# Performance work log

Measured on AMD Instinct MI355X. Metric: run time of the kernel, lower is better.

Reference implementation:

```python
import jax, jax.numpy as jnp
import numpy as np


def setup_inputs() -> dict:
    key = jax.random.key(0)
    ks = jax.random.split(key, 12)
    b, c, h, w = 2, 128, 256, 512          # x: [b,c,h,w], h == d_model
    n_cond, d_cond, d_attn = 512, 512, 256  # single head: d_attn = n_heads*d_head = 256
    return {
        "x": jax.random.normal(ks[0], (b, c, h, w), jnp.float32),
        "v": jax.random.normal(ks[1], (b, n_cond, d_cond), jnp.float32),
        "Wq": jax.random.normal(ks[2], (h, d_attn), jnp.float32) * 0.05,
        "Wk": jax.random.normal(ks[3], (d_cond, d_attn), jnp.float32) * 0.05,
        "Wv": jax.random.normal(ks[4], (d_cond, d_attn), jnp.float32) * 0.05,
        "Wo": jax.random.normal(ks[5], (d_attn, h), jnp.float32) * 0.05,
        "bo": jnp.zeros((h,), jnp.float32),
        "mask_w": jax.random.normal(ks[6], (h,), jnp.float32),  # ConvTranspose2d(1,1,(1,h)) weight, applied to ones -> just the kernel
        "conv_w": jax.random.normal(ks[7], (c, 2 * c, 3, 3), jnp.float32) * 0.02,
        "conv_b": jnp.zeros((c,), jnp.float32),
        "gn_gamma": jnp.ones((c,), jnp.float32),
        "gn_beta": jnp.zeros((c,), jnp.float32),
    }


def reference(x, v, Wq, Wk, Wv, Wo, bo, mask_w, conv_w, conv_b, gn_gamma, gn_beta):
    b, c, h, w = x.shape
    # ---- CrossAttention (note: self.scale defined but never applied in source) ----
    xt = jnp.swapaxes(x, 2, 3)                        # [b,c,w,h]
    q = jnp.einsum("bcwh,hd->bcwd", xt, Wq)           # [b,c,w,d_attn]
    k = jnp.einsum("bnd,de->bne", v, Wk)              # [b,n_cond,d_attn]
    val = jnp.einsum("bnd,de->bne", v, Wv)
    attn = jnp.einsum("bcwd,bnd->bcwn", q, k)         # [b,c,w,n_cond]
    attn = jax.nn.softmax(attn, axis=-1)
    out = jnp.einsum("bcwn,bnd->bcwd", attn, val)     # [b,c,w,d_attn]
    out = jnp.einsum("bcwd,dh->bcwh", out, Wo) + bo   # [b,c,w,h]
    attn_feature = jnp.swapaxes(out, 2, 3)            # [b,c,h,w]

    # ---- NonAdaptiveLearnedMask (eval mode: no Gaussian noise) ----
    sig = jax.nn.sigmoid(mask_w)                      # [h]
    x2 = jnp.broadcast_to(sig[None, :], (b, h))       # [b,h]
    k_keep = int(h * (1.0 - 0.2))                     # p=0.2 hardcoded in module
    topval = jax.lax.top_k(x2, k_keep)[0][:, -1:]     # kth-largest per row [b,1]
    comp = (x2 >= topval).astype(x2.dtype)
    wta = comp * x2                                   # sparsified sigmoid outputs
    slope = 1.0
    probs = jax.nn.sigmoid(slope * wta)
    hard = (probs > 0.5).astype(x2.dtype)             # straight-through binary act
    binary = probs + jax.lax.stop_gradient(hard - probs)  # [b,h]
    binary_mask = jnp.broadcast_to(binary[:, None, None, :], (b, 1, w, h))
    masked_x = jnp.swapaxes(binary_mask * jnp.swapaxes(x, 2, 3), 2, 3)  # [b,c,h,w]

    # ---- conv3x3 on concat + GroupNorm + SiLU ----
    cat = jnp.concatenate([masked_x, attn_feature], axis=1)  # [b,2c,h,w]
    hh = jax.lax.conv_general_dilated(
        cat, conv_w, window_strides=(1, 1), padding="SAME",
        dimension_numbers=("NCHW", "OIHW", "NCHW"))
    hh = hh + conv_b[None, :, None, None]
    g = min(c // 4, 32)
    hr = hh.reshape(b, g, c // g, h, w)
    mean = hr.mean(axis=(2, 3, 4), keepdims=True)
    var = hr.var(axis=(2, 3, 4), keepdims=True)
    hn = ((hr - mean) * jax.lax.rsqrt(var + 1e-6)).reshape(b, c, h, w)
    hn = hn * gn_gamma[None, :, None, None] + gn_beta[None, :, None, None]
    out = hn * jax.nn.sigmoid(hn)  # SiLU
    return (out, binary_mask)
```

## Files before the change

### kernel.cpp

```cpp
#include <hip/hip_runtime.h>
#include <math.h>

#define B      2
#define C      128
#define H      256
#define W      512
#define NCOND  512
#define DCOND  512
#define DATTN  256
#define KKEEP  204

#define WS_CATN   0ull
#define WS_KQ     134742016ull
#define WS_VOT    135266304ull
#define WS_W9     135790592ull
#define WS_BIN    136380416ull
#define WS_ST2    136381440ull

typedef __attribute__((ext_vector_type(8))) short bf16x8;
typedef __attribute__((ext_vector_type(4))) float f32x4;

union U8 { bf16x8 v; ushort u[8]; };

__device__ inline ushort f2bf(float f) {
    union { float f; unsigned u; } v; v.f = f;
    unsigned r = v.u + 0x7fffu + ((v.u >> 16) & 1u);
    return (ushort)(r >> 16);
}

__device__ __forceinline__ void gld16(const ushort* g, void* l) {
    __builtin_amdgcn_global_load_lds(
        (const __attribute__((address_space(1))) unsigned int*)(const void*)g,
        (__attribute__((address_space(3))) unsigned int*)l, 16, 0, 0);
}

__global__ void k_binary(const float* __restrict__ mask_w, float* __restrict__ bin) {
    __shared__ float s[H];
    int t = threadIdx.x;
    float sv = 1.0f / (1.0f + __expf(-mask_w[t]));
    s[t] = sv;
    __syncthreads();
    int cnt = 0;
    for (int j = 0; j < H; ++j) cnt += (s[j] > sv) ? 1 : 0;
    bin[t] = (cnt < KKEEP) ? 1.0f : 0.0f;
}

__global__ void k_maskout(const float* __restrict__ bin, float* __restrict__ mout) {
    int i = blockIdx.x * 256 + threadIdx.x;
    if (i < B * W * H) mout[i] = bin[i & (H - 1)];
}

__launch_bounds__(256)
__global__ void k_kv(const float* __restrict__ v, const float* __restrict__ Wk,
                     const float* __restrict__ Wv, const float* __restrict__ Wq,
                     const float* __restrict__ Wo, ushort* __restrict__ kq16,
                     ushort* __restrict__ voT16) {
    __shared__ float vrow[DCOND];
    __shared__ float kld[DATTN];
    __shared__ float vld[DATTN];
    int bn = blockIdx.x;
    int t  = threadIdx.x;
    const float* vp = v + (size_t)bn * DCOND;
    for (int i = t; i < DCOND; i += 256) vrow[i] = vp[i];
    __syncthreads();
    float ka = 0.f, va = 0.f;
    for (int d4 = 0; d4 < DCOND / 4; ++d4) {
        float4 vv = *(const float4*)(vrow + d4 * 4);
        const float* wk = Wk + (d4 * 4) * DATTN + t;
        const float* wv = Wv + (d4 * 4) * DATTN + t;
        ka += vv.x * wk[0];         va += vv.x * wv[0];
        ka += vv.y * wk[DATTN];     va += vv.y * wv[DATTN];
        ka += vv.z * wk[2 * DATTN]; va += vv.z * wv[2 * DATTN];
        ka += vv.w * wk[3 * DATTN]; va += vv.w * wv[3 * DATTN];
    }
    kld[t] = ka; vld[t] = va;
    __syncthreads();
    float kq = 0.f;
    const float4* wqr = (const float4*)(Wq + (size_t)t * DATTN);
#pragma unroll 8
    for (int d4 = 0; d4 < DATTN / 4; ++d4) {
        float4 w = wqr[d4];
        kq += kld[d4 * 4] * w.x + kld[d4 * 4 + 1] * w.y
            + kld[d4 * 4 + 2] * w.z + kld[d4 * 4 + 3] * w.w;
    }
    float vo = 0.f;
#pragma unroll 8
    for (int d = 0; d < DATTN; ++d) vo += vld[d] * Wo[(size_t)d * 256 + t];
    kq16[(size_t)bn * 256 + t] = f2bf(kq);
    int b = bn >> 9, n = bn & 511;
    voT16[((size_t)b * 256 + t) * 512 + n] = f2bf(vo);
}

__global__ void k_w9p(const float* __restrict__ cw, ushort* __restrict__ w9p) {
    int i = blockIdx.x * 256 + threadIdx.x;
    if (i >= 294912) return;
    int cp = i >> 13;
    int r  = i & 8191;
    int co = r >> 6;
    int u  = r & 63;
    int us = u >> 3, j = u & 7;
    int c  = cp / 9, p = cp - c * 9;
    int cc = ((us ^ (co & 7)) << 3) | j;
    int ci = c * 64 + cc;
    w9p[(size_t)cp * 8192 + co * 64 + u] = f2bf(cw[(co * 256 + ci) * 9 + p]);
}

__launch_bounds__(256)
__global__ void k_attn(const float* __restrict__ x, const ushort* __restrict__ kq16,
                       const ushort* __restrict__ voT16, const float* __restrict__ bo,
                       ushort* __restrict__ af16) {
    __shared__ __align__(16) char arena[33792];
    float* smax = (float*)(arena + 32768);
    float* ssum = (float*)(arena + 33280);

    const int t   = threadIdx.x;
    const int blk = blockIdx.x;
    const int b   = blk >> 11;
    const int ci  = (blk >> 4) & 127;
    const int w0  = (blk & 15) << 5;
    const int wid = t >> 6;
    const int lr  = t & 15;
    const int lg  = (t & 63) >> 4;

    {
        const float* xp = x + (((size_t)b * C + ci) * H + t) * W + w0;
#pragma unroll
        for (int j4 = 0; j4 < 8; ++j4) {
            float4 v4 = *(const float4*)(xp + j4 * 4);
            int j = j4 * 4;
            *(ushort*)(arena + (j + 0) * 512 + ((2 * t) ^ (((j + 0) & 7) << 4))) = f2bf(v4.x);
            *(ushort*)(arena + (j + 1) * 512 + ((2 * t) ^ (((j + 1) & 7) << 4))) = f2bf(v4.y);
            *(ushort*)(arena + (j + 2) * 512 + ((2 * t) ^ (((j + 2) & 7) << 4))) = f2bf(v4.z);
            *(ushort*)(arena + (j + 3) * 512 + ((2 * t) ^ (((j + 3) & 7) << 4))) = f2bf(v4.w);
        }
    }
    __syncthreads();

    float rinv[2][4];
    {
        f32x4 sac[2][8];
#pragma unroll
        for (int mb = 0; mb < 2; ++mb)
#pragma unroll
            for (int nb = 0; nb < 8; ++nb) sac[mb][nb] = (f32x4){0.f, 0.f, 0.f, 0.f};
        const ushort* kqb = kq16 + (size_t)b * (NCOND * DATTN);
        for (int ks = 0; ks < 8; ++ks) {
            int kb = (ks * 64 + lg * 16) ^ ((lr & 7) << 4);
            bf16x8 a0 = *(const bf16x8*)(arena + lr * 512 + kb);
            bf16x8 a1 = *(const bf16x8*)(arena + (16 + lr) * 512 + kb);
            const ushort* kp = kqb + ks * 32 + lg * 8;
#pragma unroll
            for (int nb = 0; nb < 8; ++nb) {
                int n = wid * 128 + nb * 16 + lr;
                bf16x8 bf = *(const bf16x8*)(kp + n * 256);
                sac[0][nb] = __builtin_amdgcn_mfma_f32_16x16x32_bf16(a0, bf, sac[0][nb], 0, 0, 0);
                sac[1][nb] = __builtin_amdgcn_mfma_f32_16x16x32_bf16(a1, bf, sac[1][nb], 0, 0, 0);
            }
        }
        float pmax[2][4];
#pragma unroll
        for (int mb = 0; mb < 2; ++mb)
#pragma unroll
            for (int r = 0; r < 4; ++r) {
                float m = sac[mb][0][r];
#pragma unroll
                for (int nb = 1; nb < 8; ++nb) m = fmaxf(m, sac[mb][nb][r]);
#pragma unroll
                for (int o = 8; o >= 1; o >>= 1) m = fmaxf(m, __shfl_xor(m, o));
                pmax[mb][r] = m;
            }
        if (lr == 0) {
#pragma unroll
            for (int mb = 0; mb < 2; ++mb)
#pragma unroll
                for (int r = 0; r < 4; ++r)
                    smax[(mb * 16 + lg * 4 + r) * 4 + wid] = pmax[mb][r];
        }
        __syncthreads();
        float psum[2][4];
#pragma unroll
        for (int mb = 0; mb < 2; ++mb)
#pragma unroll
            for (int r = 0; r < 4; ++r) {
                int m = mb * 16 + lg * 4 + r;
                float g = fmaxf(fmaxf(smax[m * 4], smax[m * 4 + 1]),
                                fmaxf(smax[m * 4 + 2], smax[m * 4 + 3]));
                float s = 0.f;
#pragma unroll
                for (int nb = 0; nb < 8; ++nb) {
                    float e = __expf(sac[mb][nb][r] - g);
                    s += e;
                    int n = wid * 128 + nb * 16 + lr;
                    *(ushort*)(arena + m * 1024 + ((2 * n) ^ ((m & 7) << 4))) = f2bf(e);
                }
#pragma unroll
                for (int o = 8; o >= 1; o >>= 1) s += __shfl_xor(s, o);
                psum[mb][r] = s;
            }
        if (lr == 0) {
#pragma unroll
            for (int mb = 0; mb < 2; ++mb)
#pragma unroll
                for (int r = 0; r < 4; ++r)
                    ssum[(mb * 16 + lg * 4 + r) * 4 + wid] = psum[mb][r];
        }
        __syncthreads();
#pragma unroll
        for (int mb = 0; mb < 2; ++mb)
#pragma unroll
            for (int r = 0; r < 4; ++r) {
                int m = mb * 16 + lg * 4 + r;
                rinv[mb][r] = 1.0f / (ssum[m * 4] + ssum[m * 4 + 1] + ssum[m * 4 + 2] + ssum[m * 4 + 3]);
            }
    }

    {
        f32x4 oac[2][4];
#pragma unroll
        for (int mb = 0; mb < 2; ++mb)
#pragma unroll
            for (int nb = 0; nb < 4; ++nb) oac[mb][nb] = (f32x4){0.f, 0.f, 0.f, 0.f};
        const ushort* vb = voT16 + (size_t)b * (DATTN * NCOND);
        for (int ks = 0; ks < 16; ++ks) {
            int kb = (ks * 64 + lg * 16) ^ ((lr & 7) << 4);
            bf16x8 a0 = *(const bf16x8*)(arena + lr * 1024 + kb);
            bf16x8 a1 = *(const bf16x8*)(arena + (16 + lr) * 1024 + kb);
            const ushort* vp = vb + ks * 32 + lg * 8;
#pragma unroll
            for (int nb = 0; nb < 4; ++nb) {
                int d = wid * 64 + nb * 16 + lr;
                bf16x8 bf = *(const bf16x8*)(vp + d * 512);
                oac[0][nb] = __builtin_amdgcn_mfma_f32_16x16x32_bf16(a0, bf, oac[0][nb], 0, 0, 0);
                oac[1][nb] = __builtin_amdgcn_mfma_f32_16x16x32_bf16(a1, bf, oac[1][nb], 0, 0, 0);
            }
        }
        size_t afbase = ((size_t)b * C + ci) * H * W;
#pragma unroll
        for (int nb = 0; nb < 4; ++nb) {
            int h = wid * 64 + nb * 16 + lr;
            float bias = bo[h];
            ushort* op = af16 + afbase + (size_t)h * W + w0;
#pragma unroll
            for (int mb = 0; mb < 2; ++mb) {
                ushort4 u;
                u.x = f2bf(oac[mb][nb][0] * rinv[mb][0] + bias);
                u.y = f2bf(oac[mb][nb][1] * rinv[mb][1] + bias);
                u.z = f2bf(oac[mb][nb][2] * rinv[mb][2] + bias);
                u.w = f2bf(oac[mb][nb][3] * rinv[mb][3] + bias);
                *(ushort4*)(op + mb * 16 + lg * 4) = u;
            }
        }
    }
}

__launch_bounds__(256)
__global__ void k_cat(const float* __restrict__ x, const ushort* __restrict__ af16,
                      const float* __restrict__ bin, ushort* __restrict__ catn) {
    __shared__ __align__(16) char st[32768];
    const int t   = threadIdx.x;
    const int blk = blockIdx.x;
    const int xt  = blk & 7;
    const int y   = (blk >> 3) & 255;
    const int b   = blk >> 11;
    const int x0  = xt * 64;
    const float bw = bin[y];

    for (int i = t; i < 2048; i += 256) {
        int cc = i >> 4, c4 = i & 15;
        float4 v = *(const float4*)(x + (((size_t)b * C + cc) * H + y) * W + x0 + c4 * 4);
#pragma unroll
        for (int j = 0; j < 4; ++j) {
            int px = c4 * 4 + j;
            float f = (j == 0 ? v.x : j == 1 ? v.y : j == 2 ? v.z : v.w) * bw;
            *(ushort*)(st + px * 512 + ((2 * cc) ^ ((px & 7) << 4))) = f2bf(f);
        }
    }
    for (int i = t; i < 1024; i += 256) {
        int cc = i >> 3, c8 = i & 7;
        U8 v;
        v.v = *(const bf16x8*)(af16 + (((size_t)b * C + cc) * H + y) * W + x0 + c8 * 8);
#pragma unroll
        for (int j = 0; j < 8; ++j) {
            int px = c8 * 8 + j;
            *(ushort*)(st + px * 512 + ((2 * (128 + cc)) ^ ((px & 7) << 4))) = v.u[j];
        }
    }
    __syncthreads();
    const size_t rowb = ((size_t)b * H + y) * 514;
    for (int i = t; i < 2048; i += 256) {
        int px = i >> 5, c16 = i & 31;
        int c = c16 >> 3, cgs = c16 & 7;
        int ix = x0 + px + 1;
        int cgl = cgs ^ (ix & 7);
        bf16x8 v = *(const bf16x8*)(st + px * 512 + ((((c << 3) | cgl) << 4) ^ ((px & 7) << 4)));
        *(bf16x8*)(catn + (rowb + ix) * 256 + c * 64 + cgs * 8) = v;
    }
    const bf16x8 z = {0, 0, 0, 0, 0, 0, 0, 0};
    if (xt == 0 && t < 32) *(bf16x8*)(catn + (rowb + 0) * 256 + t * 8) = z;
    if (xt == 7 && t < 32) *(bf16x8*)(catn + (rowb + 513) * 256 + t * 8) = z;
}

__launch_bounds__(512, 4)
__global__ void k_convg(const ushort* __restrict__ catn, const ushort* __restrict__ w9p,
                        const float* __restrict__ conv_b, float* __restrict__ out,
                        float* __restrict__ pb) {
    __shared__ __align__(16) char stf[55296];
    __shared__ __align__(16) char wls[16384];
    __shared__ float pst[4][64];
    const int t   = threadIdx.x;
    const int ln  = t & 63;
    const int blk = blockIdx.x;
    const int xt  = blk & 7;
    const int yq  = (blk >> 3) & 63;
    const int b   = blk >> 9;
    const int x0  = xt * 64;
    const int y0  = yq * 4;
    const int wid = t >> 6;
    const int wm  = wid >> 1;
    const int wn  = wid & 1;
    const int lr  = t & 15;
    const int lg  = (t & 63) >> 4;
    const ushort* cbase = catn + (size_t)b * ((size_t)H * 514 * 256);

    f32x4 acc[4][4];
#pragma unroll
    for (int mb = 0; mb < 4; ++mb)
#pragma unroll
        for (int nb = 0; nb < 4; ++nb) acc[mb][nb] = (f32x4){0.f, 0.f, 0.f, 0.f};

    for (int c = 0; c < 4; ++c) {
        __syncthreads();
        for (int q = wid; q < 54; q += 8) {
            int r = q / 9, seg = q - r * 9;
            int iy = y0 - 1 + r;
            char* ldsb = stf + r * 9216 + seg * 1024;
            if ((unsigned)iy < (unsigned)H) {
                const ushort* src = cbase + ((size_t)iy * 514 + x0 + seg * 8 + (ln >> 3)) * 256
                                  + c * 64 + (ln & 7) * 8;
                gld16(src, ldsb);
            } else {
                *(f32x4*)(ldsb + ln * 16) = (f32x4){0.f, 0.f, 0.f, 0.f};
            }
        }
        {
            const ushort* wsrc = w9p + (size_t)(c * 9 + 0) * 8192;
#pragma unroll
            for (int q = wid * 2; q < wid * 2 + 2; ++q)
                gld16(wsrc + q * 512 + ln * 8, wls + q * 1024);
        }
        __syncthreads();

        for (int p = 0; p < 9; ++p) {
            const int dy = p / 3, dx = p - dy * 3;
            const char* arow = stf + (wm + dy) * 9216;
#pragma unroll
            for (int ks = 0; ks < 2; ++ks) {
                bf16x8 afr[4];
#pragma unroll
                for (int mb = 0; mb < 4; ++mb) {
                    int px = mb * 16 + lr + dx;
                    afr[mb] = *(const bf16x8*)(arow + px * 128 + ((ks * 64 + lg * 16) ^ ((px & 7) << 4)));
                }
                bf16x8 bfr[4];
#pragma unroll
                for (int nb = 0; nb < 4; ++nb) {
                    int co = wn * 64 + nb * 16 + lr;
                    bfr[nb] = *(const bf16x8*)(wls + co * 128 + ((ks * 64 + lg * 16) ^ ((co & 7) << 4)));
                }
#pragma unroll
                for (int nb = 0; nb < 4; ++nb)
#pragma unroll
                    for (int mb = 0; mb < 4; ++mb)
                        acc[mb][nb] = __builtin_amdgcn_mfma_f32_16x16x32_bf16(afr[mb], bfr[nb], acc[mb][nb], 0, 0, 0);
            }
            if (p < 8) {
                __syncthreads();
                const ushort* wsrc = w9p + (size_t)(c * 9 + p + 1) * 8192;
#pragma unroll
                for (int q = wid * 2; q < wid * 2 + 2; ++q)
                    gld16(wsrc + q * 512 + ln * 8, wls + q * 1024);
                __syncthreads();
            }
        }
    }

#pragma unroll
    for (int nb = 0; nb < 4; ++nb) {
        int co = wn * 64 + nb * 16 + lr;
        float bias = conv_b[co];
        float s = 0.f, ss = 0.f;
        float* op = out + (((size_t)b * C + co) * H + (y0 + wm)) * W + x0;
#pragma unroll
        for (int mb = 0; mb < 4; ++mb) {
            float4 o = make_float4(acc[mb][nb][0] + bias, acc[mb][nb][1] + bias,
                                   acc[mb][nb][2] + bias, acc[mb][nb][3] + bias);
            s  += (o.x + o.y) + (o.z + o.w);
            ss += (o.x * o.x + o.y * o.y) + (o.z * o.z + o.w * o.w);
            *(float4*)(op + mb * 16 + lg * 4) = o;
        }
        s += __shfl_xor(s, 1);  ss += __shfl_xor(ss, 1);
        s += __shfl_xor(s, 2);  ss += __shfl_xor(ss, 2);
        s += __shfl_xor(s, 16); ss += __shfl_xor(ss, 16);
        s += __shfl_xor(s, 32); ss += __shfl_xor(ss, 32);
        if (lg == 0 && (lr & 3) == 0) {
            int g = co >> 2;
            pst[wm][g * 2]     = s;
            pst[wm][g * 2 + 1] = ss;
        }
    }
    __syncthreads();
    if (t < 64)
        pb[(size_t)blk * 64 + t] = pst[0][t] + pst[1][t] + pst[2][t] + pst[3][t];
}

__global__ void k_stats2(const float* __restrict__ pb, float* __restrict__ st2) {
    __shared__ float red[512];
    int blk = blockIdx.x;
    int b = blk >> 5, g = blk & 31;
    int t = threadIdx.x;
    float s = 0.f, ss = 0.f;
    for (int j = t; j < 512; j += 256) {
        const float* p = pb + ((size_t)(b * 512 + j)) * 64 + g * 2;
        s += p[0]; ss += p[1];
    }
    red[t * 2] = s; red[t * 2 + 1] = ss;
    __syncthreads();
    for (int o = 128; o >= 1; o >>= 1) {
        if (t < o) {
            red[t * 2]     += red[(t + o) * 2];
            red[t * 2 + 1] += red[(t + o) * 2 + 1];
        }
        __syncthreads();
    }
    if (t == 0) {
        const float inv = 1.0f / 524288.0f;
        float mean = red[0] * inv;
        float var  = red[1] * inv - mean * mean;
        st2[blk * 2]     = mean;
        st2[blk * 2 + 1] = rsqrtf(var + 1e-6f);
    }
}

__global__ void k_norm(const float* __restrict__ st2, const float* __restrict__ gamma,
                       const float* __restrict__ beta, float* __restrict__ out) {
    const int N4 = B * C * H * W / 4;
    int stride = gridDim.x * 256;
    for (int i4 = blockIdx.x * 256 + threadIdx.x; i4 < N4; i4 += stride) {
        int i = i4 * 4;
        int c = (i >> 17) & 127;
        int b = i >> 24;
        int g = c >> 2;
        float mean = st2[(b * 32 + g) * 2];
        float rstd = st2[(b * 32 + g) * 2 + 1];
        float ga = gamma[c], be = beta[c];
        float4 v = *(float4*)(out + i);
        float n0 = (v.x - mean) * rstd * ga + be;
        float n1 = (v.y - mean) * rstd * ga + be;
        float n2 = (v.z - mean) * rstd * ga + be;
        float n3 = (v.w - mean) * rstd * ga + be;
        v.x = n0 / (1.0f + __expf(-n0));
        v.y = n1 / (1.0f + __expf(-n1));
        v.z = n2 / (1.0f + __expf(-n2));
        v.w = n3 / (1.0f + __expf(-n3));
        *(float4*)(out + i) = v;
    }
}

extern "C" void kernel_launch(void* const* d_in, const int* in_sizes, int n_in,
                              void* d_out, int out_size, void* d_ws, size_t ws_size,
                              hipStream_t stream) {
    const float* x      = (const float*)d_in[0];
    const float* v      = (const float*)d_in[1];
    const float* Wq     = (const float*)d_in[2];
    const float* Wk     = (const float*)d_in[3];
    const float* Wv     = (const float*)d_in[4];
    const float* Wo     = (const float*)d_in[5];
    const float* bo     = (const float*)d_in[6];
    const float* mask_w = (const float*)d_in[7];
    const float* conv_w = (const float*)d_in[8];
    const float* conv_b = (const float*)d_in[9];
    const float* gng    = (const float*)d_in[10];
    const float* gnb    = (const float*)d_in[11];

    float* out  = (float*)d_out;
    float* mout = out + B * C * H * W;
    ushort* af16 = (ushort*)d_out;

    char*  wsb  = (char*)d_ws;
    ushort* catn  = (ushort*)(wsb + WS_CATN);
    ushort* kq16  = (ushort*)(wsb + WS_KQ);
    ushort* voT16 = (ushort*)(wsb + WS_VOT);
    ushort* w9p   = (ushort*)(wsb + WS_W9);
    float*  bin   = (float*)(wsb + WS_BIN);
    float*  st2   = (float*)(wsb + WS_ST2);
    float*  pb    = (float*)(wsb + WS_KQ);

    k_binary <<<1,    256, 0, stream>>>(mask_w, bin);
    k_maskout<<<1024, 256, 0, stream>>>(bin, mout);
    k_kv     <<<B * NCOND, 256, 0, stream>>>(v, Wk, Wv, Wq, Wo, kq16, voT16);
    k_w9p    <<<1152, 256, 0, stream>>>(conv_w, w9p);
    k_attn   <<<4096, 256, 0, stream>>>(x, kq16, voT16, bo, af16);
    k_cat    <<<4096, 256, 0, stream>>>(x, af16, bin, catn);
    k_convg  <<<1024, 512, 0, stream>>>(catn, w9p, conv_b, out, pb);
    k_stats2 <<<64,   256, 0, stream>>>(pb, st2);
    k_norm   <<<2048, 256, 0, stream>>>(st2, gng, gnb, out);
}
```

Measured before the change: 601.5 us.

## Stage KQ and VO operands through swizzled LDS tiles in attention kernel

The attention kernel used to read its B operands (kq and voT) straight from global memory with strided per-lane loads. The KV-producing kernel now writes them in a chunked, XOR-swizzled layout, and each attention block copies 32KB chunks into a new LDS buffer with gld16 before reading them conflict-free for the MFMAs. This targets poorly coalesced global reads. In exchange it adds a 32KB LDS buffer per block, which may lower occupancy, and two barriers per chunk.

```diff
diff --git a/kernel.cpp b/kernel.cpp
--- a/kernel.cpp
+++ b/kernel.cpp
@@ -53,8 +53,8 @@
 __launch_bounds__(256)
 __global__ void k_kv(const float* __restrict__ v, const float* __restrict__ Wk,
                      const float* __restrict__ Wv, const float* __restrict__ Wq,
-                     const float* __restrict__ Wo, ushort* __restrict__ kq16,
-                     ushort* __restrict__ voT16) {
+                     const float* __restrict__ Wo, ushort* __restrict__ kqc,
+                     ushort* __restrict__ voc) {
     __shared__ float vrow[DCOND];
     __shared__ float kld[DATTN];
     __shared__ float vld[DATTN];
@@ -86,9 +86,19 @@
     float vo = 0.f;
 #pragma unroll 8
     for (int d = 0; d < DATTN; ++d) vo += vld[d] * Wo[(size_t)d * 256 + t];
-    kq16[(size_t)bn * 256 + t] = f2bf(kq);
+
     int b = bn >> 9, n = bn & 511;
-    voT16[((size_t)b * 256 + t) * 512 + n] = f2bf(vo);
+    {
+        int s    = ((t >> 6) << 1) | (n >> 8);
+        int nl   = n & 255;
+        int slot = (((t >> 3) & 7) ^ (n & 7));
+        kqc[(((size_t)(b * 8 + s)) * 256 + nl) * 64 + slot * 8 + (t & 7)] = f2bf(kq);
+    }
+    {
+        int s2   = n >> 6;
+        int slot = (((n >> 3) & 7) ^ (t & 7));
+        voc[(((size_t)(b * 8 + s2)) * 256 + t) * 64 + slot * 8 + (n & 7)] = f2bf(vo);
+    }
 }
 
 __global__ void k_w9p(const float* __restrict__ cw, ushort* __restrict__ w9p) {
@@ -106,14 +116,16 @@
 }
 
 __launch_bounds__(256)
-__global__ void k_attn(const float* __restrict__ x, const ushort* __restrict__ kq16,
-                       const ushort* __restrict__ voT16, const float* __restrict__ bo,
+__global__ void k_attn(const float* __restrict__ x, const ushort* __restrict__ kqc,
+                       const ushort* __restrict__ voc, const float* __restrict__ bo,
                        ushort* __restrict__ af16) {
     __shared__ __align__(16) char arena[33792];
+    __shared__ __align__(16) char bbuf[32768];
     float* smax = (float*)(arena + 32768);
     float* ssum = (float*)(arena + 33280);
 
     const int t   = threadIdx.x;
+    const int ln  = t & 63;
     const int blk = blockIdx.x;
     const int b   = blk >> 11;
     const int ci  = (blk >> 4) & 127;
@@ -134,7 +146,6 @@
             *(ushort*)(arena + (j + 3) * 512 + ((2 * t) ^ (((j + 3) & 7) << 4))) = f2bf(v4.w);
         }
     }
-    __syncthreads();
 
     float rinv[2][4];
     {
@@ -142,19 +153,32 @@
 #pragma unroll
         for (int mb = 0; mb < 2; ++mb)
 #pragma unroll
-            for (int nb = 0; nb < 8; ++nb) sac[mb][nb] = (f32x4){0.f, 0.f, 0.f, 0.f};
-        const ushort* kqb = kq16 + (size_t)b * (NCOND * DATTN);
-        for (int ks = 0; ks < 8; ++ks) {
-            int kb = (ks * 64 + lg * 16) ^ ((lr & 7) << 4);
-            bf16x8 a0 = *(const bf16x8*)(arena + lr * 512 + kb);
-            bf16x8 a1 = *(const bf16x8*)(arena + (16 + lr) * 512 + kb);
-            const ushort* kp = kqb + ks * 32 + lg * 8;
-#pragma unroll
-            for (int nb = 0; nb < 8; ++nb) {
-                int n = wid * 128 + nb * 16 + lr;
-                bf16x8 bf = *(const bf16x8*)(kp + n * 256);
-                sac[0][nb] = __builtin_amdgcn_mfma_f32_16x16x32_bf16(a0, bf, sac[0][nb], 0, 0, 0);
-                sac[1][nb] = __builtin_amdgcn_mfma_f32_16x16x32_bf16(a1, bf, sac[1][nb], 0, 0, 0);
+            for (int g = 0; g < 8; ++g) sac[mb][g] = (f32x4){0.f, 0.f, 0.f, 0.f};
+        const ushort* kqb = kqc + (size_t)b * 131072;
+        for (int s = 0; s < 8; ++s) {
+            __syncthreads();
+            const ushort* src = kqb + s * 16384;
+#pragma unroll
+            for (int i = 0; i < 8; ++i) {
+                int q = wid * 8 + i;
+                gld16(src + q * 512 + ln * 8, bbuf + q * 1024);
+            }
+            __syncthreads();
+#pragma unroll
+            for (int ksl = 0; ksl < 2; ++ksl) {
+                int gks = (s >> 1) * 2 + ksl;
+                int kb = (gks * 64 + lg * 16) ^ ((lr & 7) << 4);
+                bf16x8 a0 = *(const bf16x8*)(arena + lr * 512 + kb);
+                bf16x8 a1 = *(const bf16x8*)(arena + (16 + lr) * 512 + kb);
+#pragma unroll
+                for (int nb = 0; nb < 4; ++nb) {
+                    int nl = wid * 64 + nb * 16 + lr;
+                    int slot = (ksl * 4 + lg) ^ (nl & 7);
+                    bf16x8 bf = *(const bf16x8*)(bbuf + nl * 128 + slot * 16);
+                    int g = (s & 1) * 4 + nb;
+                    sac[0][g] = __builtin_amdgcn_mfma_f32_16x16x32_bf16(a0, bf, sac[0][g], 0, 0, 0);
+                    sac[1][g] = __builtin_amdgcn_mfma_f32_16x16x32_bf16(a1, bf, sac[1][g], 0, 0, 0);
+                }
             }
         }
         float pmax[2][4];
@@ -164,7 +188,7 @@
             for (int r = 0; r < 4; ++r) {
                 float m = sac[mb][0][r];
 #pragma unroll
-                for (int nb = 1; nb < 8; ++nb) m = fmaxf(m, sac[mb][nb][r]);
+                for (int g = 1; g < 8; ++g) m = fmaxf(m, sac[mb][g][r]);
 #pragma unroll
                 for (int o = 8; o >= 1; o >>= 1) m = fmaxf(m, __shfl_xor(m, o));
                 pmax[mb][r] = m;
@@ -183,14 +207,14 @@
 #pragma unroll
             for (int r = 0; r < 4; ++r) {
                 int m = mb * 16 + lg * 4 + r;
-                float g = fmaxf(fmaxf(smax[m * 4], smax[m * 4 + 1]),
-                                fmaxf(smax[m * 4 + 2], smax[m * 4 + 3]));
+                float g2 = fmaxf(fmaxf(smax[m * 4], smax[m * 4 + 1]),
+                                 fmaxf(smax[m * 4 + 2], smax[m * 4 + 3]));
                 float s = 0.f;
 #pragma unroll
-                for (int nb = 0; nb < 8; ++nb) {
-                    float e = __expf(sac[mb][nb][r] - g);
+                for (int g = 0; g < 8; ++g) {
+                    float e = __expf(sac[mb][g][r] - g2);
                     s += e;
-                    int n = wid * 128 + nb * 16 + lr;
+                    int n = (g >> 2) * 256 + wid * 64 + (g & 3) * 16 + lr;
                     *(ushort*)(arena + m * 1024 + ((2 * n) ^ ((m & 7) << 4))) = f2bf(e);
                 }
 #pragma unroll
@@ -220,18 +244,30 @@
         for (int mb = 0; mb < 2; ++mb)
 #pragma unroll
             for (int nb = 0; nb < 4; ++nb) oac[mb][nb] = (f32x4){0.f, 0.f, 0.f, 0.f};
-        const ushort* vb = voT16 + (size_t)b * (DATTN * NCOND);
-        for (int ks = 0; ks < 16; ++ks) {
-            int kb = (ks * 64 + lg * 16) ^ ((lr & 7) << 4);
-            bf16x8 a0 = *(const bf16x8*)(arena + lr * 1024 + kb);
-            bf16x8 a1 = *(const bf16x8*)(arena + (16 + lr) * 1024 + kb);
-            const ushort* vp = vb + ks * 32 + lg * 8;
-#pragma unroll
-            for (int nb = 0; nb < 4; ++nb) {
-                int d = wid * 64 + nb * 16 + lr;
-                bf16x8 bf = *(const bf16x8*)(vp + d * 512);
-                oac[0][nb] = __builtin_amdgcn_mfma_f32_16x16x32_bf16(a0, bf, oac[0][nb], 0, 0, 0);
-                oac[1][nb] = __builtin_amdgcn_mfma_f32_16x16x32_bf16(a1, bf, oac[1][nb], 0, 0, 0);
+        const ushort* vob = voc + (size_t)b * 131072;
+        for (int s2 = 0; s2 < 8; ++s2) {
+            __syncthreads();
+            const ushort* src = vob + s2 * 16384;
+#pragma unroll
+            for (int i = 0; i < 8; ++i) {
+                int q = wid * 8 + i;
+                gld16(src + q * 512 + ln * 8, bbuf + q * 1024);
+            }
+            __syncthreads();
+#pragma unroll
+            for (int ksl = 0; ksl < 2; ++ksl) {
+                int gks = s2 * 2 + ksl;
+                int kb = (gks * 64 + lg * 16) ^ ((lr & 7) << 4);
+                bf16x8 a0 = *(const bf16x8*)(arena + lr * 1024 + kb);
+                bf16x8 a1 = *(const bf16x8*)(arena + (16 + lr) * 1024 + kb);
+#pragma unroll
+                for (int nb = 0; nb < 4; ++nb) {
+                    int d = wid * 64 + nb * 16 + lr;
+                    int slot = (ksl * 4 + lg) ^ (d & 7);
+                    bf16x8 bf = *(const bf16x8*)(bbuf + d * 128 + slot * 16);
+                    oac[0][nb] = __builtin_amdgcn_mfma_f32_16x16x32_bf16(a0, bf, oac[0][nb], 0, 0, 0);
+                    oac[1][nb] = __builtin_amdgcn_mfma_f32_16x16x32_bf16(a1, bf, oac[1][nb], 0, 0, 0);
+                }
             }
         }
         size_t afbase = ((size_t)b * C + ci) * H * W;
@@ -488,8 +524,8 @@
 
     char*  wsb  = (char*)d_ws;
     ushort* catn  = (ushort*)(wsb + WS_CATN);
-    ushort* kq16  = (ushort*)(wsb + WS_KQ);
-    ushort* voT16 = (ushort*)(wsb + WS_VOT);
+    ushort* kqc   = (ushort*)(wsb + WS_KQ);
+    ushort* voc   = (ushort*)(wsb + WS_VOT);
     ushort* w9p   = (ushort*)(wsb + WS_W9);
     float*  bin   = (float*)(wsb + WS_BIN);
     float*  st2   = (float*)(wsb + WS_ST2);
@@ -497,9 +533,9 @@
 
     k_binary <<<1,    256, 0, stream>>>(mask_w, bin);
     k_maskout<<<1024, 256, 0, stream>>>(bin, mout);
-    k_kv     <<<B * NCOND, 256, 0, stream>>>(v, Wk, Wv, Wq, Wo, kq16, voT16);
+    k_kv     <<<B * NCOND, 256, 0, stream>>>(v, Wk, Wv, Wq, Wo, kqc, voc);
     k_w9p    <<<1152, 256, 0, stream>>>(conv_w, w9p);
-    k_attn   <<<4096, 256, 0, stream>>>(x, kq16, voT16, bo, af16);
+    k_attn   <<<4096, 256, 0, stream>>>(x, kqc, voc, bo, af16);
     k_cat    <<<4096, 256, 0, stream>>>(x, af16, bin, catn);
     k_convg  <<<1024, 512, 0, stream>>>(catn, w9p, conv_b, out, pb);
     k_stats2 <<<64,   256, 0, stream>>>(pb, st2);
```

Result: faster. 509.1 us (-15.4%).
